# Performance work log

Hardware: AMD Instinct MI355X
Metric: run time of the kernel (lower is better)

## Reference

```python
import jax, jax.numpy as jnp
import numpy as np

B, S, E = 2048, 23, 768
RED, H, NUM_LABELS = 256, 8, 25
DH = RED // H
DELTA = 0.1
EPS_LN = 1e-5


def setup_inputs() -> dict:
    key = jax.random.key(0)
    ks = jax.random.split(key, 20)
    g = lambda k, shape, fan: jax.random.normal(k, shape, dtype=jnp.float32) * (1.0 / np.sqrt(fan))
    inp = {
        'cls_embeddings': jax.random.normal(ks[0], (B, S, E), dtype=jnp.float32),
        'existing_mask': jax.random.randint(ks[1], (B, S), 0, 2, dtype=jnp.int32),
        'missing_emb': g(ks[2], (S, E), E),
        'W1': g(ks[3], (E // 2, E), E), 'b1': jnp.zeros((E // 2,), jnp.float32),
        'W2': g(ks[4], (RED, E // 2), E // 2), 'b2': jnp.zeros((RED,), jnp.float32),
        'ln_g': jnp.ones((RED,), jnp.float32), 'ln_b': jnp.zeros((RED,), jnp.float32),
        'Wq': g(ks[5], (RED, RED), RED), 'bq': jnp.zeros((RED,), jnp.float32),
        'Wk': g(ks[6], (RED, RED), RED), 'bk': jnp.zeros((RED,), jnp.float32),
        'Wv': g(ks[7], (RED, RED), RED), 'bv': jnp.zeros((RED,), jnp.float32),
        'Wo': g(ks[8], (RED, RED), RED), 'bo': jnp.zeros((RED,), jnp.float32),
        'Wp': g(ks[9], (NUM_LABELS, RED), RED), 'bp': jnp.zeros((NUM_LABELS,), jnp.float32),
    }
    return inp


def _layer_norm(x, g, b):
    mu = jnp.mean(x, axis=-1, keepdims=True)
    var = jnp.mean(jnp.square(x - mu), axis=-1, keepdims=True)
    return (x - mu) * jax.lax.rsqrt(var + EPS_LN) * g + b


def _forward(cls_embeddings, existing_mask, missing_emb, W1, b1, W2, b2, ln_g, ln_b,
             Wq, bq, Wk, bk, Wv, bv, Wo, bo, Wp, bp):
    exist = existing_mask > 0                              # [B,S] bool
    # Gather: existing sections use BERT CLS, missing slots use learned embeddings
    sec = jnp.where(exist[..., None], cls_embeddings, missing_emb[None])  # [B,S,E]
    # SectionDimReducer (exact-erf GELU as in nn.GELU default)
    h = jax.nn.gelu(sec @ W1.T + b1, approximate=False)
    h = jax.nn.gelu(h @ W2.T + b2, approximate=False)
    red = _layer_norm(h, ln_g, ln_b)                       # [B,S,RED]
    # Tiny MHA: every slot queries the existing sections of its own EHR
    q = (red @ Wq.T + bq).reshape(B, S, H, DH)
    k = (red @ Wk.T + bk).reshape(B, S, H, DH)
    v = (red @ Wv.T + bv).reshape(B, S, H, DH)
    scores = jnp.einsum('bqhd,bkhd->bhqk', q, k) / np.sqrt(DH)
    scores = jnp.where(exist[:, None, None, :], scores, -1e9)
    attn = jax.nn.softmax(scores, axis=-1)                 # [B,H,S,S]
    ctx = jnp.einsum('bhqk,bkhd->bqhd', attn, v).reshape(B, S, RED)
    mha_out = ctx @ Wo.T + bo                              # [B,S,RED]
    # Scatter: only missing slots (of EHRs with >=1 existing section) are replaced
    any_exist = jnp.any(exist, axis=1)                     # [B]
    use_attn = (~exist) & any_exist[:, None]               # [B,S]
    updated = jnp.where(use_attn[..., None], mha_out, red)
    # margin-based orthogonality loss on section embeddings
    norm = updated / jnp.maximum(jnp.linalg.norm(updated, axis=-1, keepdims=True), 1e-8)
    gram = jnp.einsum('bid,bjd->bij', norm, norm)          # [B,S,S]
    off = 1.0 - jnp.eye(S, dtype=updated.dtype)
    loss_orth = jnp.sum(jax.nn.relu(jnp.abs(gram) - DELTA) * off) / (B * S * (S - 1))
    logits = updated.mean(axis=1) @ Wp.T + bp              # [B,NUM_LABELS]
    return loss_orth, logits


def reference(cls_embeddings, existing_mask, missing_emb, W1, b1, W2, b2, ln_g, ln_b,
              Wq, bq, Wk, bk, Wv, bv, Wo, bo, Wp, bp):
    return _forward(cls_embeddings, existing_mask, missing_emb, W1, b1, W2, b2, ln_g, ln_b,
                    Wq, bq, Wk, bk, Wv, bv, Wo, bo, Wp, bp)
```

## Files before the change

kernel.cpp:

```cpp
#include <hip/hip_runtime.h>

typedef unsigned short u16;
typedef unsigned int u32;
typedef __attribute__((ext_vector_type(8))) short short8;
typedef __attribute__((ext_vector_type(4))) float f32x4;

struct __align__(8) us4 { u16 x, y, z, w; };

__device__ __forceinline__ float bf1(u16 v){ return __uint_as_float(((u32)v) << 16); }
__device__ __forceinline__ float bflo(u32 u){ return __uint_as_float(u << 16); }
__device__ __forceinline__ float bfhi(u32 u){ return __uint_as_float(u & 0xFFFF0000u); }
__device__ __forceinline__ u16 fbf(float f){
    u32 u = __float_as_uint(f);
    return (u16)((u + 0x7FFFu + ((u >> 16) & 1u)) >> 16);
}
__device__ __forceinline__ float gelu_exact(float x){
    return 0.5f * x * (1.0f + erff(x * 0.70710678118654752f));
}
__device__ __forceinline__ void unp8(uint4 u, float* f){
    f[0]=bflo(u.x); f[1]=bfhi(u.x); f[2]=bflo(u.y); f[3]=bfhi(u.y);
    f[4]=bflo(u.z); f[5]=bfhi(u.z); f[6]=bflo(u.w); f[7]=bfhi(u.w);
}
__device__ __forceinline__ uint4 pack8(float4 a, float4 b){
    uint4 u;
    u.x = (u32)fbf(a.x) | ((u32)fbf(a.y) << 16);
    u.y = (u32)fbf(a.z) | ((u32)fbf(a.w) << 16);
    u.z = (u32)fbf(b.x) | ((u32)fbf(b.y) << 16);
    u.w = (u32)fbf(b.z) | ((u32)fbf(b.w) << 16);
    return u;
}

#define MFMA16(a, b, c) __builtin_amdgcn_mfma_f32_16x16x32_bf16(a, b, c, 0, 0, 0)
#define QSTR 264
#define CAPROWS 46208


__global__ __launch_bounds__(256) void wconv(
    const float* __restrict__ W1, const float* __restrict__ W2,
    const float* __restrict__ Wq, const float* __restrict__ Wk,
    const float* __restrict__ Wv, const float* __restrict__ Wo,
    const float* __restrict__ Wp, u16* __restrict__ dst)
{
    const int i = blockIdx.x * 256 + threadIdx.x;
    const float* s; int o;
    if      (i < 294912) { s = W1; o = i; }
    else if (i < 393216) { s = W2; o = i - 294912; }
    else if (i < 458752) { s = Wq; o = i - 393216; }
    else if (i < 524288) { s = Wk; o = i - 458752; }
    else if (i < 589824) { s = Wv; o = i - 524288; }
    else if (i < 655360) { s = Wo; o = i - 589824; }
    else                 { s = Wp; o = i - 655360; }
    dst[i] = fbf(s[o]);
}

__global__ __launch_bounds__(256) void scan_kernel(
    const int* __restrict__ mask, int* __restrict__ idx,
    int* __restrict__ rowsrc, int* __restrict__ cnt)
{
    const int i = blockIdx.x * 256 + threadIdx.x;
    if (blockIdx.x == 0 && threadIdx.x < 23)
        rowsrc[threadIdx.x] = -(threadIdx.x + 1);
    if (mask[i] > 0) {
        const int slot = 23 + atomicAdd(cnt, 1);
        idx[i] = slot;
        rowsrc[slot] = i;
    }
}

__global__ __launch_bounds__(256) void gemm1_kernel(
    const float* __restrict__ cls, const int* __restrict__ rowsrc,
    const int* __restrict__ cnt, const float* __restrict__ missing,
    const u16* __restrict__ W, const float* __restrict__ bias,
    u16* __restrict__ C)
{
    const int K = 768, M = 384;
    const int nBase = blockIdx.y * 128;
    if (nBase >= *cnt + 23) return;
    __shared__ u16 As[128 * 40];
    __shared__ u16 Bs[128 * 40];
    const int tid = threadIdx.x;
    const int w = tid >> 6, lane = tid & 63;
    const int mBase = blockIdx.x * 128;
    const int wr = w >> 1, wc = w & 1;
    const int r0 = tid >> 2;
    const int co = (tid & 3) * 8;
    const int frow = lane & 15, quad = lane >> 4;

    const int rs0 = rowsrc[nBase + r0];
    const int rs1 = rowsrc[nBase + r0 + 64];
    const float* ap0 = (rs0 >= 0) ? cls + (size_t)rs0 * 768
                                  : missing + (size_t)(-rs0 - 1) * 768;
    const float* ap1 = (rs1 >= 0) ? cls + (size_t)rs1 * 768
                                  : missing + (size_t)(-rs1 - 1) * 768;
    const u16* bp0 = W + (size_t)(mBase + r0) * K;
    const u16* bp1 = W + (size_t)(mBase + r0 + 64) * K;

    f32x4 acc[4][4];
#pragma unroll
    for (int mt = 0; mt < 4; ++mt)
#pragma unroll
        for (int nt = 0; nt < 4; ++nt) acc[mt][nt] = f32x4{0.f, 0.f, 0.f, 0.f};

    float4 a0a = *(const float4*)(ap0 + co), a0b = *(const float4*)(ap0 + co + 4);
    float4 a1a = *(const float4*)(ap1 + co), a1b = *(const float4*)(ap1 + co + 4);
    uint4 pb0 = *(const uint4*)(bp0 + co), pb1 = *(const uint4*)(bp1 + co);

    for (int k0 = 0; k0 < K; k0 += 32) {
        __syncthreads();
        *(uint4*)(As + r0 * 40 + co) = pack8(a0a, a0b);
        *(uint4*)(As + (r0 + 64) * 40 + co) = pack8(a1a, a1b);
        *(uint4*)(Bs + r0 * 40 + co) = pb0;
        *(uint4*)(Bs + (r0 + 64) * 40 + co) = pb1;
        __syncthreads();
        if (k0 + 32 < K) {
            const int kn = k0 + 32 + co;
            a0a = *(const float4*)(ap0 + kn); a0b = *(const float4*)(ap0 + kn + 4);
            a1a = *(const float4*)(ap1 + kn); a1b = *(const float4*)(ap1 + kn + 4);
            pb0 = *(const uint4*)(bp0 + kn);  pb1 = *(const uint4*)(bp1 + kn);
        }
        short8 af[4], bfv[4];
#pragma unroll
        for (int mt = 0; mt < 4; ++mt)
            af[mt] = *(const short8*)(As + (wr * 64 + mt * 16 + frow) * 40 + quad * 8);
#pragma unroll
        for (int nt = 0; nt < 4; ++nt)
            bfv[nt] = *(const short8*)(Bs + (wc * 64 + nt * 16 + frow) * 40 + quad * 8);
#pragma unroll
        for (int mt = 0; mt < 4; ++mt)
#pragma unroll
            for (int nt = 0; nt < 4; ++nt)
                acc[mt][nt] = MFMA16(af[mt], bfv[nt], acc[mt][nt]);
    }

#pragma unroll
    for (int nt = 0; nt < 4; ++nt) {
        const int col = mBase + wc * 64 + nt * 16 + frow;
        const float bv = bias[col];
#pragma unroll
        for (int mt = 0; mt < 4; ++mt)
#pragma unroll
            for (int reg = 0; reg < 4; ++reg) {
                const int row = nBase + wr * 64 + mt * 16 + quad * 4 + reg;
                C[(size_t)row * M + col] = fbf(gelu_exact(acc[mt][nt][reg] + bv));
            }
    }
}

__global__ __launch_bounds__(256) void gemm_bt(
    const u16* __restrict__ A, const u16* __restrict__ W,
    const float* __restrict__ bias, u16* __restrict__ C, int K, int M,
    const int* __restrict__ cnt)
{
    const int nBase = blockIdx.y * 128;
    if (nBase >= *cnt + 23) return;
    __shared__ u16 As[128 * 40];
    __shared__ u16 Bs[128 * 40];
    const int tid = threadIdx.x;
    const int w = tid >> 6, lane = tid & 63;
    const int mBase = blockIdx.x * 128;
    const int wr = w >> 1, wc = w & 1;
    const int r0 = tid >> 2;
    const int co = (tid & 3) * 8;
    const int frow = lane & 15, quad = lane >> 4;

    f32x4 acc[4][4];
#pragma unroll
    for (int mt = 0; mt < 4; ++mt)
#pragma unroll
        for (int nt = 0; nt < 4; ++nt) acc[mt][nt] = f32x4{0.f, 0.f, 0.f, 0.f};

    uint4 pa0 = *(const uint4*)(A + (size_t)(nBase + r0) * K + co);
    uint4 pa1 = *(const uint4*)(A + (size_t)(nBase + r0 + 64) * K + co);
    uint4 pb0 = *(const uint4*)(W + (size_t)(mBase + r0) * K + co);
    uint4 pb1 = *(const uint4*)(W + (size_t)(mBase + r0 + 64) * K + co);

    for (int k0 = 0; k0 < K; k0 += 32) {
        __syncthreads();
        *(uint4*)(As + r0 * 40 + co) = pa0;
        *(uint4*)(As + (r0 + 64) * 40 + co) = pa1;
        *(uint4*)(Bs + r0 * 40 + co) = pb0;
        *(uint4*)(Bs + (r0 + 64) * 40 + co) = pb1;
        __syncthreads();
        if (k0 + 32 < K) {
            const int kn = k0 + 32 + co;
            pa0 = *(const uint4*)(A + (size_t)(nBase + r0) * K + kn);
            pa1 = *(const uint4*)(A + (size_t)(nBase + r0 + 64) * K + kn);
            pb0 = *(const uint4*)(W + (size_t)(mBase + r0) * K + kn);
            pb1 = *(const uint4*)(W + (size_t)(mBase + r0 + 64) * K + kn);
        }
        short8 af[4], bfv[4];
#pragma unroll
        for (int mt = 0; mt < 4; ++mt)
            af[mt] = *(const short8*)(As + (wr * 64 + mt * 16 + frow) * 40 + quad * 8);
#pragma unroll
        for (int nt = 0; nt < 4; ++nt)
            bfv[nt] = *(const short8*)(Bs + (wc * 64 + nt * 16 + frow) * 40 + quad * 8);
#pragma unroll
        for (int mt = 0; mt < 4; ++mt)
#pragma unroll
            for (int nt = 0; nt < 4; ++nt)
                acc[mt][nt] = MFMA16(af[mt], bfv[nt], acc[mt][nt]);
    }

#pragma unroll
    for (int nt = 0; nt < 4; ++nt) {
        const int col = mBase + wc * 64 + nt * 16 + frow;
        const float bv = bias[col];
#pragma unroll
        for (int mt = 0; mt < 4; ++mt)
#pragma unroll
            for (int reg = 0; reg < 4; ++reg) {
                const int row = nBase + wr * 64 + mt * 16 + quad * 4 + reg;
                C[(size_t)row * M + col] = fbf(gelu_exact(acc[mt][nt][reg] + bv));
            }
    }
}

__device__ __forceinline__ void ln1_reg(
    const float* x, const float4& g0, const float4& g1,
    const float4& b0, const float4& b1, u16* rp)
{
    float s = x[0] + x[1] + x[2] + x[3] + x[4] + x[5] + x[6] + x[7];
    s += __shfl_xor(s, 1); s += __shfl_xor(s, 2); s += __shfl_xor(s, 4);
    s += __shfl_xor(s, 8); s += __shfl_xor(s, 16);
    const float mu = s * (1.f / 256.f);
    float v = 0.f;
#pragma unroll
    for (int e = 0; e < 8; ++e) { const float d = x[e] - mu; v += d * d; }
    v += __shfl_xor(v, 1); v += __shfl_xor(v, 2); v += __shfl_xor(v, 4);
    v += __shfl_xor(v, 8); v += __shfl_xor(v, 16);
    const float rs = rsqrtf(v * (1.f / 256.f) + 1e-5f);
    float4 ya, yb;
    ya.x = (x[0]-mu)*rs*g0.x + b0.x;
    ya.y = (x[1]-mu)*rs*g0.y + b0.y;
    ya.z = (x[2]-mu)*rs*g0.z + b0.z;
    ya.w = (x[3]-mu)*rs*g0.w + b0.w;
    yb.x = (x[4]-mu)*rs*g1.x + b1.x;
    yb.y = (x[5]-mu)*rs*g1.y + b1.y;
    yb.z = (x[6]-mu)*rs*g1.z + b1.z;
    yb.w = (x[7]-mu)*rs*g1.w + b1.w;
    *(uint4*)rp = pack8(ya, yb);
}

__device__ __forceinline__ void ln3_reg_store(
    uint4 rg0, uint4 rg1, uint4 rg2, bool has2,
    const float* __restrict__ lng, const float* __restrict__ lnb,
    u16* dstBase, int s0, int c0o)
{
    const float4 g0 = *(const float4*)(lng + c0o);
    const float4 g1 = *(const float4*)(lng + c0o + 4);
    const float4 b0 = *(const float4*)(lnb + c0o);
    const float4 b1 = *(const float4*)(lnb + c0o + 4);
    float x[8];
    unp8(rg0, x); ln1_reg(x, g0, g1, b0, b1, dstBase + s0 * QSTR + c0o);
    unp8(rg1, x); ln1_reg(x, g0, g1, b0, b1, dstBase + (s0 + 8) * QSTR + c0o);
    if (has2) { unp8(rg2, x); ln1_reg(x, g0, g1, b0, b1, dstBase + (s0 + 16) * QSTR + c0o); }
}

#define KLOOP_PF(WPTR, SRC, ACC)                                                  \
    {                                                                             \
        short8 nb0 = *(const short8*)(WPTR);                                      \
        short8 nb1 = *(const short8*)((WPTR) + 16 * 256);                         \
        short8 nb2 = *(const short8*)((WPTR) + 32 * 256);                         \
        short8 nb3 = *(const short8*)((WPTR) + 48 * 256);                         \
        for (int k0 = 0; k0 < 256; k0 += 32) {                                    \
            short8 a0 = *(const short8*)((SRC) + r0c * QSTR + k0 + quad * 8);     \
            short8 a1 = *(const short8*)((SRC) + r1c * QSTR + k0 + quad * 8);     \
            short8 c0 = nb0, c1 = nb1, c2 = nb2, c3 = nb3;                        \
            if (k0 + 32 < 256) {                                                  \
                nb0 = *(const short8*)((WPTR) + (k0 + 32));                       \
                nb1 = *(const short8*)((WPTR) + 16 * 256 + (k0 + 32));            \
                nb2 = *(const short8*)((WPTR) + 32 * 256 + (k0 + 32));            \
                nb3 = *(const short8*)((WPTR) + 48 * 256 + (k0 + 32));            \
            }                                                                     \
            ACC[0][0] = MFMA16(a0, c0, ACC[0][0]); ACC[1][0] = MFMA16(a1, c0, ACC[1][0]); \
            ACC[0][1] = MFMA16(a0, c1, ACC[0][1]); ACC[1][1] = MFMA16(a1, c1, ACC[1][1]); \
            ACC[0][2] = MFMA16(a0, c2, ACC[0][2]); ACC[1][2] = MFMA16(a1, c2, ACC[1][2]); \
            ACC[0][3] = MFMA16(a0, c3, ACC[0][3]); ACC[1][3] = MFMA16(a1, c3, ACC[1][3]); \
        }                                                                         \
    }

__global__ __launch_bounds__(256, 3) void attn_tail_kernel(
    const u16* __restrict__ redb, const int* __restrict__ mask,
    const int* __restrict__ idxArr,
    const u16* __restrict__ Wqkvb,
    const float* __restrict__ bq, const float* __restrict__ bk,
    const float* __restrict__ bv, const u16* __restrict__ Wob,
    const float* __restrict__ bo, const float* __restrict__ lng,
    const float* __restrict__ lnb, const u16* __restrict__ Wpb,
    const float* __restrict__ bp, float* __restrict__ out,
    float* __restrict__ lossAcc)
{
    __shared__ __align__(16) unsigned char SM[40960];
    u16* s_rq = (u16*)SM;
    u16* s_k  = (u16*)(SM + 12144);
    u16* s_vT = (u16*)(SM + 24288);
    int* sEx   = (int*)(SM + 40672);
    int* sMiss = (int*)(SM + 40764);
    int* sCrow = (int*)(SM + 40856);
    float* sDiag = (float*)(SM + 24288);
    float* sInv  = (float*)(SM + 24384);
    float* sPool = (float*)(SM + 24480);

    const int b = blockIdx.x, t = threadIdx.x;
    const int w = t >> 6, lane = t & 63;
    const int frow = lane & 15, quad = lane >> 4;
    const int r0c = frow;
    const int r1c = (16 + frow > 22) ? 22 : 16 + frow;
    const f32x4 z4 = f32x4{0.f, 0.f, 0.f, 0.f};

    {
        const int myEx = (t < 23) ? mask[b * 23 + t] : 0;
        if (t < 23) {
            sEx[t] = myEx;
            sCrow[t] = (myEx > 0) ? idxArr[b * 23 + t] : t;
        }
        if (t < 64) {
            const unsigned long long ball = __ballot((t < 23) && (myEx > 0));
            if (t < 23) sMiss[t] = (ball != 0ull && myEx <= 0) ? 1 : 0;
        }
    }
    for (int i = t; i < 1024; i += 256) ((uint4*)s_vT)[i] = make_uint4(0u, 0u, 0u, 0u);
    __syncthreads();

    {
        const int s0 = t >> 5, c0o = (t & 31) * 8;
        uint4 rg0 = *(const uint4*)(redb + (size_t)sCrow[s0] * 256 + c0o);
        uint4 rg1 = *(const uint4*)(redb + (size_t)sCrow[s0 + 8] * 256 + c0o);
        uint4 rg2 = make_uint4(0u, 0u, 0u, 0u);
        const bool has2 = t < 224;
        if (has2) rg2 = *(const uint4*)(redb + (size_t)sCrow[s0 + 16] * 256 + c0o);
        ln3_reg_store(rg0, rg1, rg2, has2, lng, lnb, s_rq, s0, c0o);
    }
    __syncthreads();

    const int cmb = w * 64 + frow;
    {
        f32x4 ka[2][4];
#pragma unroll
        for (int mt = 0; mt < 2; ++mt)
#pragma unroll
            for (int nt = 0; nt < 4; ++nt) ka[mt][nt] = z4;
        const u16* wp = Wqkvb + (size_t)(256 + cmb) * 256 + quad * 8;
        const float bb[4] = {bk[cmb], bk[cmb + 16], bk[cmb + 32], bk[cmb + 48]};
        KLOOP_PF(wp, s_rq, ka)
#pragma unroll
        for (int nt = 0; nt < 4; ++nt) {
            const int cm = cmb + nt * 16;
#pragma unroll
            for (int mt = 0; mt < 2; ++mt)
#pragma unroll
                for (int reg = 0; reg < 4; ++reg) {
                    const int s = mt * 16 + quad * 4 + reg;
                    if (s < 23) s_k[s * QSTR + cm] = fbf(ka[mt][nt][reg] + bb[nt]);
                }
        }
    }
    {
        f32x4 va[2][4];
#pragma unroll
        for (int mt = 0; mt < 2; ++mt)
#pragma unroll
            for (int nt = 0; nt < 4; ++nt) va[mt][nt] = z4;
        const u16* wp = Wqkvb + (size_t)(512 + cmb) * 256 + quad * 8;
        const float bb[4] = {bv[cmb], bv[cmb + 16], bv[cmb + 32], bv[cmb + 48]};
        KLOOP_PF(wp, s_rq, va)
#pragma unroll
        for (int nt = 0; nt < 4; ++nt) {
            const int cm = cmb + nt * 16;
#pragma unroll
            for (int mt = 0; mt < 2; ++mt)
#pragma unroll
                for (int reg = 0; reg < 4; ++reg) {
                    const int s = mt * 16 + quad * 4 + reg;
                    if (s < 23) s_vT[cm * 32 + s] = fbf(va[mt][nt][reg] + bb[nt]);
                }
        }
    }
    {
        f32x4 qa[2][4];
#pragma unroll
        for (int mt = 0; mt < 2; ++mt)
#pragma unroll
            for (int nt = 0; nt < 4; ++nt) qa[mt][nt] = z4;
        const u16* wp = Wqkvb + (size_t)cmb * 256 + quad * 8;
        const float bb[4] = {bq[cmb], bq[cmb + 16], bq[cmb + 32], bq[cmb + 48]};
        KLOOP_PF(wp, s_rq, qa)
        __syncthreads();
#pragma unroll
        for (int nt = 0; nt < 4; ++nt) {
            const int cm = cmb + nt * 16;
#pragma unroll
            for (int mt = 0; mt < 2; ++mt)
#pragma unroll
                for (int reg = 0; reg < 4; ++reg) {
                    const int s = mt * 16 + quad * 4 + reg;
                    if (s < 23) s_rq[s * QSTR + cm] = fbf(qa[mt][nt][reg] + bb[nt]);
                }
        }
    }

    {
        const float scl = 0.17677669529663687f;
        const float m0 = (sEx[frow] > 0) ? 0.f : -1e9f;
        const float m1 = (16 + frow < 23 && sEx[16 + frow] > 0) ? 0.f : -1e9f;
#pragma unroll
        for (int hh2 = 0; hh2 < 2; ++hh2) {
            const int hb = w * 64 + hh2 * 32;
            short8 aq0 = *(const short8*)(s_rq + r0c * QSTR + hb + quad * 8);
            short8 aq1 = *(const short8*)(s_rq + r1c * QSTR + hb + quad * 8);
            short8 bk0 = *(const short8*)(s_k + r0c * QSTR + hb + quad * 8);
            short8 bk1 = *(const short8*)(s_k + r1c * QSTR + hb + quad * 8);
            f32x4 s00 = MFMA16(aq0, bk0, z4);
            f32x4 s01 = MFMA16(aq0, bk1, z4);
            f32x4 s10 = MFMA16(aq1, bk0, z4);
            f32x4 s11 = MFMA16(aq1, bk1, z4);
#pragma unroll
            for (int mt = 0; mt < 2; ++mt) {
                f32x4& c0 = mt ? s10 : s00;
                f32x4& c1 = mt ? s11 : s01;
#pragma unroll
                for (int reg = 0; reg < 4; ++reg) {
                    float v0 = c0[reg] * scl + m0;
                    float v1 = c1[reg] * scl + m1;
                    float mx = fmaxf(v0, v1);
#pragma unroll
                    for (int m = 8; m; m >>= 1) mx = fmaxf(mx, __shfl_xor(mx, m));
                    float p0 = __expf(v0 - mx), p1 = __expf(v1 - mx);
                    float sm = p0 + p1;
#pragma unroll
                    for (int m = 8; m; m >>= 1) sm += __shfl_xor(sm, m);
                    const float inv = 1.f / sm;
                    c0[reg] = p0 * inv;
                    c1[reg] = p1 * inv;
                }
            }
#pragma unroll
            for (int reg = 0; reg < 4; ++reg) {
                const int q0r = quad * 4 + reg;
                s_k[q0r * QSTR + hb + frow]      = fbf(s00[reg]);
                s_k[q0r * QSTR + hb + 16 + frow] = fbf(s01[reg]);
                const int q1r = 16 + quad * 4 + reg;
                if (q1r < 23) {
                    s_k[q1r * QSTR + hb + frow]      = fbf(s10[reg]);
                    s_k[q1r * QSTR + hb + 16 + frow] = fbf(s11[reg]);
                }
            }
            short8 pa0 = *(const short8*)(s_k + r0c * QSTR + hb + quad * 8);
            short8 pa1 = *(const short8*)(s_k + r1c * QSTR + hb + quad * 8);
            short8 bv0 = *(const short8*)(s_vT + (hb + frow) * 32 + quad * 8);
            short8 bv1 = *(const short8*)(s_vT + (hb + 16 + frow) * 32 + quad * 8);
            f32x4 c00 = MFMA16(pa0, bv0, z4);
            f32x4 c01 = MFMA16(pa0, bv1, z4);
            f32x4 c10 = MFMA16(pa1, bv0, z4);
            f32x4 c11 = MFMA16(pa1, bv1, z4);
#pragma unroll
            for (int reg = 0; reg < 4; ++reg) {
                const int q0r = quad * 4 + reg;
                s_rq[q0r * QSTR + hb + frow]      = fbf(c00[reg]);
                s_rq[q0r * QSTR + hb + 16 + frow] = fbf(c01[reg]);
                const int q1r = 16 + quad * 4 + reg;
                if (q1r < 23) {
                    s_rq[q1r * QSTR + hb + frow]      = fbf(c10[reg]);
                    s_rq[q1r * QSTR + hb + 16 + frow] = fbf(c11[reg]);
                }
            }
        }
    }
    __syncthreads();

    {
        f32x4 wacc[2][4];
#pragma unroll
        for (int mt = 0; mt < 2; ++mt)
#pragma unroll
            for (int nt = 0; nt < 4; ++nt) wacc[mt][nt] = z4;
        const u16* wp = Wob + (size_t)cmb * 256 + quad * 8;
        const float ob[4] = {bo[cmb], bo[cmb + 16], bo[cmb + 32], bo[cmb + 48]};
        KLOOP_PF(wp, s_rq, wacc)
        {
            const int s0 = t >> 5, c0o = (t & 31) * 8;
            uint4 rg0 = *(const uint4*)(redb + (size_t)sCrow[s0] * 256 + c0o);
            uint4 rg1 = *(const uint4*)(redb + (size_t)sCrow[s0 + 8] * 256 + c0o);
            uint4 rg2 = make_uint4(0u, 0u, 0u, 0u);
            const bool has2 = t < 224;
            if (has2) rg2 = *(const uint4*)(redb + (size_t)sCrow[s0 + 16] * 256 + c0o);
            ln3_reg_store(rg0, rg1, rg2, has2, lng, lnb, s_k, s0, c0o);
        }
        __syncthreads();
#pragma unroll
        for (int nt = 0; nt < 4; ++nt) {
            const int col = cmb + nt * 16;
#pragma unroll
            for (int mt = 0; mt < 2; ++mt)
#pragma unroll
                for (int reg = 0; reg < 4; ++reg) {
                    const int s = mt * 16 + quad * 4 + reg;
                    if (s < 23 && sMiss[s])
                        s_k[s * QSTR + col] = fbf(wacc[mt][nt][reg] + ob[nt]);
                }
        }
    }
    __syncthreads();

    f32x4 g00 = z4, g01 = z4, g10 = z4, g11 = z4;
    if (w == 0) {
        short8 ga0 = *(const short8*)(s_k + r0c * QSTR + quad * 8);
        short8 ga1 = *(const short8*)(s_k + r1c * QSTR + quad * 8);
        for (int k0 = 0; k0 < 256; k0 += 32) {
            short8 a0 = ga0, a1 = ga1;
            if (k0 + 32 < 256) {
                ga0 = *(const short8*)(s_k + r0c * QSTR + k0 + 32 + quad * 8);
                ga1 = *(const short8*)(s_k + r1c * QSTR + k0 + 32 + quad * 8);
            }
            g00 = MFMA16(a0, a0, g00);
            g01 = MFMA16(a0, a1, g01);
            g10 = MFMA16(a1, a0, g10);
            g11 = MFMA16(a1, a1, g11);
        }
#pragma unroll
        for (int reg = 0; reg < 4; ++reg) {
            if (frow == quad * 4 + reg) {
                sDiag[frow] = g00[reg];
                if (16 + frow < 23) sDiag[16 + frow] = g11[reg];
            }
        }
    } else {
        for (int c = t - 64; c < 256; c += 192) {
            float pv = 0.f;
#pragma unroll
            for (int s = 0; s < 23; ++s) pv += bf1(s_k[s * QSTR + c]);
            sPool[c] = pv * (1.f / 23.f);
        }
    }
    __syncthreads();
    if (t < 23) sInv[t] = 1.f / fmaxf(sqrtf(sDiag[t]), 1e-8f);
    __syncthreads();

    if (w == 0) {
        float contrib = 0.f;
        const float ic0 = sInv[frow];
        const float ic1 = (16 + frow < 23) ? sInv[16 + frow] : 0.f;
        const bool c1ok = (16 + frow < 23);
#pragma unroll
        for (int reg = 0; reg < 4; ++reg) {
            const int rA = quad * 4 + reg;
            const float irA = sInv[rA];
            if (rA != frow) {
                const float cc = fabsf(g00[reg] * irA * ic0) - 0.1f;
                if (cc > 0.f) contrib += cc;
            }
            if (c1ok) {
                const float cc = fabsf(g01[reg] * irA * ic1) - 0.1f;
                if (cc > 0.f) contrib += cc;
            }
            const int rB = 16 + quad * 4 + reg;
            if (rB < 23) {
                const float irB = sInv[rB];
                {
                    const float cc = fabsf(g10[reg] * irB * ic0) - 0.1f;
                    if (cc > 0.f) contrib += cc;
                }
                if (c1ok && rB != 16 + frow) {
                    const float cc = fabsf(g11[reg] * irB * ic1) - 0.1f;
                    if (cc > 0.f) contrib += cc;
                }
            }
        }
#pragma unroll
        for (int m = 32; m; m >>= 1) contrib += __shfl_xor(contrib, m);
        if (lane == 0) atomicAdd(lossAcc, contrib);
    } else {
        const int li = t - 64;
        {
            const int L = li >> 3, chunk = li & 7;
            float a = 0.f;
#pragma unroll
            for (int q4 = 0; q4 < 4; ++q4) {
                const int c8 = chunk * 4 + q4;
                float wf[8]; unp8(*(const uint4*)(Wpb + (size_t)L * 256 + c8 * 8), wf);
                const float4 p0 = *(const float4*)(sPool + c8 * 8);
                const float4 p1 = *(const float4*)(sPool + c8 * 8 + 4);
                a += wf[0] * p0.x + wf[1] * p0.y + wf[2] * p0.z + wf[3] * p0.w
                   + wf[4] * p1.x + wf[5] * p1.y + wf[6] * p1.z + wf[7] * p1.w;
            }
            a += __shfl_xor(a, 1); a += __shfl_xor(a, 2); a += __shfl_xor(a, 4);
            if (chunk == 0) out[1 + b * 25 + L] = a + bp[L];
        }
        if (li < 8) {
            float a = 0.f;
#pragma unroll
            for (int q4 = 0; q4 < 4; ++q4) {
                const int c8 = li * 4 + q4;
                float wf[8]; unp8(*(const uint4*)(Wpb + (size_t)24 * 256 + c8 * 8), wf);
                const float4 p0 = *(const float4*)(sPool + c8 * 8);
                const float4 p1 = *(const float4*)(sPool + c8 * 8 + 4);
                a += wf[0] * p0.x + wf[1] * p0.y + wf[2] * p0.z + wf[3] * p0.w
                   + wf[4] * p1.x + wf[5] * p1.y + wf[6] * p1.z + wf[7] * p1.w;
            }
            a += __shfl_xor(a, 1); a += __shfl_xor(a, 2); a += __shfl_xor(a, 4);
            if (li == 0) out[1 + b * 25 + 24] = a + bp[24];
        }
    }
}

__global__ void loss_finalize(const float* __restrict__ lossAcc, float* __restrict__ out)
{
    out[0] = lossAcc[0] * (1.f / 1036288.f);
}

extern "C" void kernel_launch(void* const* d_in, const int* in_sizes, int n_in,
                              void* d_out, int out_size, void* d_ws, size_t ws_size,
                              hipStream_t stream)
{
    const float* cls     = (const float*)d_in[0];
    const int*   mask    = (const int*)d_in[1];
    const float* missing = (const float*)d_in[2];
    const float* W1 = (const float*)d_in[3];  const float* b1 = (const float*)d_in[4];
    const float* W2 = (const float*)d_in[5];  const float* b2 = (const float*)d_in[6];
    const float* lng = (const float*)d_in[7]; const float* lnb = (const float*)d_in[8];
    const float* Wq = (const float*)d_in[9];  const float* bq = (const float*)d_in[10];
    const float* Wk = (const float*)d_in[11]; const float* bk = (const float*)d_in[12];
    const float* Wv = (const float*)d_in[13]; const float* bv = (const float*)d_in[14];
    const float* Wo = (const float*)d_in[15]; const float* bo = (const float*)d_in[16];
    const float* Wp = (const float*)d_in[17]; const float* bp = (const float*)d_in[18];
    float* out = (float*)d_out;

    char* ws = (char*)d_ws;
    u16* h1b  = (u16*)ws;
    u16* redb = (u16*)(ws + 35487744);
    u16* Wb   = (u16*)(ws + 59146240);
    u16* W1b   = Wb;
    u16* W2b   = Wb + 294912;
    u16* Wqkvb = Wb + 393216;
    u16* Wob   = Wb + 589824;
    u16* Wpb   = Wb + 655360;
    int* idx    = (int*)(ws + 60469760);
    int* rowsrc = (int*)(ws + 60658176);
    int* cnt    = (int*)(ws + 60843008);
    float* lossAcc = (float*)(ws + 60843012);

    hipMemsetAsync(lossAcc, 0, sizeof(float), stream);
    hipMemsetAsync(cnt, 0, sizeof(int), stream);
    hipMemsetAsync(rowsrc, 0, CAPROWS * sizeof(int), stream);

    wconv<<<2585, 256, 0, stream>>>(W1, W2, Wq, Wk, Wv, Wo, Wp, Wb);
    scan_kernel<<<184, 256, 0, stream>>>(mask, idx, rowsrc, cnt);
    gemm1_kernel<<<dim3(3, 361), 256, 0, stream>>>(cls, rowsrc, cnt, missing,
                                                   W1b, b1, h1b);
    gemm_bt<<<dim3(2, 361), 256, 0, stream>>>(h1b, W2b, b2, redb, 384, 256, cnt);
    attn_tail_kernel<<<2048, 256, 0, stream>>>(redb, mask, idx, Wqkvb, bq, bk, bv,
                                               Wob, bo, lng, lnb, Wpb, bp,
                                               out, lossAcc);
    loss_finalize<<<1, 1, 0, stream>>>(lossAcc, out);
}
```

Baseline: 507.5 us.

## Fuse both reducer MLP GEMMs into one kernel keeping hidden activations in LDS

Merges the two dimension-reducer GEMM kernels into a single kernel. Each block takes 64 gathered rows, computes the full 384-wide first layer with GELU into shared memory, then runs the second GEMM from LDS and writes only the 256-wide output. This removes the global round trip of the intermediate activations and one launch. The trade-off is that weight fragments are now read straight from global/L2 per MFMA instead of being staged in shared memory, each block recomputes against the whole weight matrices, and the large LDS footprint may limit occupancy.

```diff
diff --git a/kernel.cpp b/kernel.cpp
--- a/kernel.cpp
+++ b/kernel.cpp
@@ -32,7 +32,8 @@
 
 #define MFMA16(a, b, c) __builtin_amdgcn_mfma_f32_16x16x32_bf16(a, b, c, 0, 0, 0)
 #define QSTR 264
-#define CAPROWS 46208
+#define CAPROWS 47232
+#define H1STR 392
 
 
 __global__ __launch_bounds__(256) void wconv(
@@ -67,153 +68,114 @@
     }
 }
 
-__global__ __launch_bounds__(256) void gemm1_kernel(
+__global__ __launch_bounds__(256) void mlp_fused(
     const float* __restrict__ cls, const int* __restrict__ rowsrc,
     const int* __restrict__ cnt, const float* __restrict__ missing,
-    const u16* __restrict__ W, const float* __restrict__ bias,
-    u16* __restrict__ C)
-{
-    const int K = 768, M = 384;
-    const int nBase = blockIdx.y * 128;
+    const u16* __restrict__ W1b, const float* __restrict__ b1,
+    const u16* __restrict__ W2b, const float* __restrict__ b2,
+    u16* __restrict__ redb)
+{
+    const int nBase = blockIdx.x * 64;
     if (nBase >= *cnt + 23) return;
-    __shared__ u16 As[128 * 40];
-    __shared__ u16 Bs[128 * 40];
+    __shared__ __align__(16) u16 h1t[64 * H1STR];
+    u16* As = h1t;
+
     const int tid = threadIdx.x;
     const int w = tid >> 6, lane = tid & 63;
-    const int mBase = blockIdx.x * 128;
     const int wr = w >> 1, wc = w & 1;
     const int r0 = tid >> 2;
     const int co = (tid & 3) * 8;
     const int frow = lane & 15, quad = lane >> 4;
+    const f32x4 z4 = f32x4{0.f, 0.f, 0.f, 0.f};
 
     const int rs0 = rowsrc[nBase + r0];
-    const int rs1 = rowsrc[nBase + r0 + 64];
     const float* ap0 = (rs0 >= 0) ? cls + (size_t)rs0 * 768
                                   : missing + (size_t)(-rs0 - 1) * 768;
-    const float* ap1 = (rs1 >= 0) ? cls + (size_t)rs1 * 768
-                                  : missing + (size_t)(-rs1 - 1) * 768;
-    const u16* bp0 = W + (size_t)(mBase + r0) * K;
-    const u16* bp1 = W + (size_t)(mBase + r0 + 64) * K;
-
-    f32x4 acc[4][4];
-#pragma unroll
-    for (int mt = 0; mt < 4; ++mt)
-#pragma unroll
-        for (int nt = 0; nt < 4; ++nt) acc[mt][nt] = f32x4{0.f, 0.f, 0.f, 0.f};
+
+    f32x4 acc[3][2][4];
+#pragma unroll
+    for (int mtile = 0; mtile < 3; ++mtile)
+#pragma unroll
+        for (int mt = 0; mt < 2; ++mt)
+#pragma unroll
+            for (int nt = 0; nt < 4; ++nt) acc[mtile][mt][nt] = z4;
 
     float4 a0a = *(const float4*)(ap0 + co), a0b = *(const float4*)(ap0 + co + 4);
-    float4 a1a = *(const float4*)(ap1 + co), a1b = *(const float4*)(ap1 + co + 4);
-    uint4 pb0 = *(const uint4*)(bp0 + co), pb1 = *(const uint4*)(bp1 + co);
-
-    for (int k0 = 0; k0 < K; k0 += 32) {
+
+    for (int k0 = 0; k0 < 768; k0 += 32) {
         __syncthreads();
         *(uint4*)(As + r0 * 40 + co) = pack8(a0a, a0b);
-        *(uint4*)(As + (r0 + 64) * 40 + co) = pack8(a1a, a1b);
-        *(uint4*)(Bs + r0 * 40 + co) = pb0;
-        *(uint4*)(Bs + (r0 + 64) * 40 + co) = pb1;
         __syncthreads();
-        if (k0 + 32 < K) {
+        if (k0 + 32 < 768) {
             const int kn = k0 + 32 + co;
             a0a = *(const float4*)(ap0 + kn); a0b = *(const float4*)(ap0 + kn + 4);
-            a1a = *(const float4*)(ap1 + kn); a1b = *(const float4*)(ap1 + kn + 4);
-            pb0 = *(const uint4*)(bp0 + kn);  pb1 = *(const uint4*)(bp1 + kn);
-        }
-        short8 af[4], bfv[4];
-#pragma unroll
-        for (int mt = 0; mt < 4; ++mt)
-            af[mt] = *(const short8*)(As + (wr * 64 + mt * 16 + frow) * 40 + quad * 8);
-#pragma unroll
-        for (int nt = 0; nt < 4; ++nt)
-            bfv[nt] = *(const short8*)(Bs + (wc * 64 + nt * 16 + frow) * 40 + quad * 8);
-#pragma unroll
-        for (int mt = 0; mt < 4; ++mt)
-#pragma unroll
-            for (int nt = 0; nt < 4; ++nt)
-                acc[mt][nt] = MFMA16(af[mt], bfv[nt], acc[mt][nt]);
-    }
-
-#pragma unroll
-    for (int nt = 0; nt < 4; ++nt) {
-        const int col = mBase + wc * 64 + nt * 16 + frow;
-        const float bv = bias[col];
-#pragma unroll
-        for (int mt = 0; mt < 4; ++mt)
-#pragma unroll
-            for (int reg = 0; reg < 4; ++reg) {
-                const int row = nBase + wr * 64 + mt * 16 + quad * 4 + reg;
-                C[(size_t)row * M + col] = fbf(gelu_exact(acc[mt][nt][reg] + bv));
-            }
-    }
-}
-
-__global__ __launch_bounds__(256) void gemm_bt(
-    const u16* __restrict__ A, const u16* __restrict__ W,
-    const float* __restrict__ bias, u16* __restrict__ C, int K, int M,
-    const int* __restrict__ cnt)
-{
-    const int nBase = blockIdx.y * 128;
-    if (nBase >= *cnt + 23) return;
-    __shared__ u16 As[128 * 40];
-    __shared__ u16 Bs[128 * 40];
-    const int tid = threadIdx.x;
-    const int w = tid >> 6, lane = tid & 63;
-    const int mBase = blockIdx.x * 128;
-    const int wr = w >> 1, wc = w & 1;
-    const int r0 = tid >> 2;
-    const int co = (tid & 3) * 8;
-    const int frow = lane & 15, quad = lane >> 4;
-
-    f32x4 acc[4][4];
-#pragma unroll
-    for (int mt = 0; mt < 4; ++mt)
-#pragma unroll
-        for (int nt = 0; nt < 4; ++nt) acc[mt][nt] = f32x4{0.f, 0.f, 0.f, 0.f};
-
-    uint4 pa0 = *(const uint4*)(A + (size_t)(nBase + r0) * K + co);
-    uint4 pa1 = *(const uint4*)(A + (size_t)(nBase + r0 + 64) * K + co);
-    uint4 pb0 = *(const uint4*)(W + (size_t)(mBase + r0) * K + co);
-    uint4 pb1 = *(const uint4*)(W + (size_t)(mBase + r0 + 64) * K + co);
-
-    for (int k0 = 0; k0 < K; k0 += 32) {
-        __syncthreads();
-        *(uint4*)(As + r0 * 40 + co) = pa0;
-        *(uint4*)(As + (r0 + 64) * 40 + co) = pa1;
-        *(uint4*)(Bs + r0 * 40 + co) = pb0;
-        *(uint4*)(Bs + (r0 + 64) * 40 + co) = pb1;
-        __syncthreads();
-        if (k0 + 32 < K) {
-            const int kn = k0 + 32 + co;
-            pa0 = *(const uint4*)(A + (size_t)(nBase + r0) * K + kn);
-            pa1 = *(const uint4*)(A + (size_t)(nBase + r0 + 64) * K + kn);
-            pb0 = *(const uint4*)(W + (size_t)(mBase + r0) * K + kn);
-            pb1 = *(const uint4*)(W + (size_t)(mBase + r0 + 64) * K + kn);
-        }
-        short8 af[4], bfv[4];
-#pragma unroll
-        for (int mt = 0; mt < 4; ++mt)
-            af[mt] = *(const short8*)(As + (wr * 64 + mt * 16 + frow) * 40 + quad * 8);
-#pragma unroll
-        for (int nt = 0; nt < 4; ++nt)
-            bfv[nt] = *(const short8*)(Bs + (wc * 64 + nt * 16 + frow) * 40 + quad * 8);
-#pragma unroll
-        for (int mt = 0; mt < 4; ++mt)
-#pragma unroll
-            for (int nt = 0; nt < 4; ++nt)
-                acc[mt][nt] = MFMA16(af[mt], bfv[nt], acc[mt][nt]);
-    }
-
-#pragma unroll
-    for (int nt = 0; nt < 4; ++nt) {
-        const int col = mBase + wc * 64 + nt * 16 + frow;
-        const float bv = bias[col];
-#pragma unroll
-        for (int mt = 0; mt < 4; ++mt)
-#pragma unroll
-            for (int reg = 0; reg < 4; ++reg) {
-                const int row = nBase + wr * 64 + mt * 16 + quad * 4 + reg;
-                C[(size_t)row * M + col] = fbf(gelu_exact(acc[mt][nt][reg] + bv));
-            }
-    }
+        }
+        short8 a0 = *(const short8*)(As + (wr * 32 + frow) * 40 + quad * 8);
+        short8 a1 = *(const short8*)(As + (wr * 32 + 16 + frow) * 40 + quad * 8);
+#pragma unroll
+        for (int mtile = 0; mtile < 3; ++mtile)
+#pragma unroll
+            for (int nt = 0; nt < 4; ++nt) {
+                const int n = mtile * 128 + wc * 64 + nt * 16 + frow;
+                short8 bfr = *(const short8*)(W1b + (size_t)n * 768 + k0 + quad * 8);
+                acc[mtile][0][nt] = MFMA16(a0, bfr, acc[mtile][0][nt]);
+                acc[mtile][1][nt] = MFMA16(a1, bfr, acc[mtile][1][nt]);
+            }
+    }
+    __syncthreads();
+
+#pragma unroll
+    for (int mtile = 0; mtile < 3; ++mtile)
+#pragma unroll
+        for (int nt = 0; nt < 4; ++nt) {
+            const int col = mtile * 128 + wc * 64 + nt * 16 + frow;
+            const float bv = b1[col];
+#pragma unroll
+            for (int mt = 0; mt < 2; ++mt)
+#pragma unroll
+                for (int reg = 0; reg < 4; ++reg) {
+                    const int row = wr * 32 + mt * 16 + quad * 4 + reg;
+                    h1t[row * H1STR + col] = fbf(gelu_exact(acc[mtile][mt][nt][reg] + bv));
+                }
+        }
+    __syncthreads();
+
+    f32x4 acc2[2][2][4];
+#pragma unroll
+    for (int mt2 = 0; mt2 < 2; ++mt2)
+#pragma unroll
+        for (int mt = 0; mt < 2; ++mt)
+#pragma unroll
+            for (int nt = 0; nt < 4; ++nt) acc2[mt2][mt][nt] = z4;
+
+    for (int k0 = 0; k0 < 384; k0 += 32) {
+        short8 a0 = *(const short8*)(h1t + (wr * 32 + frow) * H1STR + k0 + quad * 8);
+        short8 a1 = *(const short8*)(h1t + (wr * 32 + 16 + frow) * H1STR + k0 + quad * 8);
+#pragma unroll
+        for (int mt2 = 0; mt2 < 2; ++mt2)
+#pragma unroll
+            for (int nt = 0; nt < 4; ++nt) {
+                const int n = mt2 * 128 + wc * 64 + nt * 16 + frow;
+                short8 bfr = *(const short8*)(W2b + (size_t)n * 384 + k0 + quad * 8);
+                acc2[mt2][0][nt] = MFMA16(a0, bfr, acc2[mt2][0][nt]);
+                acc2[mt2][1][nt] = MFMA16(a1, bfr, acc2[mt2][1][nt]);
+            }
+    }
+
+#pragma unroll
+    for (int mt2 = 0; mt2 < 2; ++mt2)
+#pragma unroll
+        for (int nt = 0; nt < 4; ++nt) {
+            const int col = mt2 * 128 + wc * 64 + nt * 16 + frow;
+            const float bv = b2[col];
+#pragma unroll
+            for (int mt = 0; mt < 2; ++mt)
+#pragma unroll
+                for (int reg = 0; reg < 4; ++reg) {
+                    const int row = nBase + wr * 32 + mt * 16 + quad * 4 + reg;
+                    redb[(size_t)row * 256 + col] = fbf(gelu_exact(acc2[mt2][mt][nt][reg] + bv));
+                }
+        }
 }
 
 __device__ __forceinline__ void ln1_reg(
@@ -627,18 +589,17 @@
     float* out = (float*)d_out;
 
     char* ws = (char*)d_ws;
-    u16* h1b  = (u16*)ws;
-    u16* redb = (u16*)(ws + 35487744);
-    u16* Wb   = (u16*)(ws + 59146240);
+    u16* redb = (u16*)ws;
+    u16* Wb   = (u16*)(ws + 24182784);
     u16* W1b   = Wb;
     u16* W2b   = Wb + 294912;
     u16* Wqkvb = Wb + 393216;
     u16* Wob   = Wb + 589824;
     u16* Wpb   = Wb + 655360;
-    int* idx    = (int*)(ws + 60469760);
-    int* rowsrc = (int*)(ws + 60658176);
-    int* cnt    = (int*)(ws + 60843008);
-    float* lossAcc = (float*)(ws + 60843012);
+    int* idx    = (int*)(ws + 25506304);
+    int* rowsrc = (int*)(ws + 25694720);
+    int* cnt    = (int*)(ws + 25883648);
+    float* lossAcc = (float*)(ws + 25883652);
 
     hipMemsetAsync(lossAcc, 0, sizeof(float), stream);
     hipMemsetAsync(cnt, 0, sizeof(int), stream);
@@ -646,9 +607,8 @@
 
     wconv<<<2585, 256, 0, stream>>>(W1, W2, Wq, Wk, Wv, Wo, Wp, Wb);
     scan_kernel<<<184, 256, 0, stream>>>(mask, idx, rowsrc, cnt);
-    gemm1_kernel<<<dim3(3, 361), 256, 0, stream>>>(cls, rowsrc, cnt, missing,
-                                                   W1b, b1, h1b);
-    gemm_bt<<<dim3(2, 361), 256, 0, stream>>>(h1b, W2b, b2, redb, 384, 256, cnt);
+    mlp_fused<<<738, 256, 0, stream>>>(cls, rowsrc, cnt, missing,
+                                       W1b, b1, W2b, b2, redb);
     attn_tail_kernel<<<2048, 256, 0, stream>>>(redb, mask, idx, Wqkvb, bq, bk, bv,
                                                Wob, bo, lng, lnb, Wpb, bp,
                                                out, lossAcc);
```

Result: slower. 523.6 us (+3.2%).
